# Kernel tuning notes

Hardware: AMD Instinct MI355X
Metric: run time of the kernel (lower is better)

## Reference

```python
import jax, jax.numpy as jnp
import numpy as np

B, T, D, H, L, OUT, FC = 256, 512, 64, 256, 2, 1, 128


def setup_inputs() -> dict:
    key = jax.random.key(0)
    ks = jax.random.split(key, 16)
    s = 1.0 / np.sqrt(H)
    u = lambda k, shape: jax.random.uniform(k, shape, jnp.float32, -s, s)
    return {
        "x": jax.random.normal(ks[0], (B, T, D), jnp.float32),
        # layer 0 LSTM params (PyTorch gate order: i, f, g, o)
        "W_ih0": u(ks[1], (4 * H, D)),
        "W_hh0": u(ks[2], (4 * H, H)),
        "b_ih0": u(ks[3], (4 * H,)),
        "b_hh0": u(ks[4], (4 * H,)),
        # layer 1 LSTM params
        "W_ih1": u(ks[5], (4 * H, H)),
        "W_hh1": u(ks[6], (4 * H, H)),
        "b_ih1": u(ks[7], (4 * H,)),
        "b_hh1": u(ks[8], (4 * H,)),
        # MLP head
        "fc1_w": u(ks[9], (FC, H)),
        "fc1_b": u(ks[10], (FC,)),
        "fc2_w": u(ks[11], (OUT, FC)),
        "fc2_b": u(ks[12], (OUT,)),
    }


def _lstm_layer(x, W_ih, W_hh, b_ih, b_hh):
    # x: [B, T, Din] -> (outputs [B, T, H], final hidden [B, H])
    Bsz = x.shape[0]
    Hh = W_hh.shape[1]
    # precompute input contribution to all gates: [B, T, 4H]
    xg = jnp.einsum("btd,gd->btg", x, W_ih) + b_ih + b_hh

    def step(carry, xt):
        h, c = carry
        g = xt + h @ W_hh.T  # [B, 4H]
        i, f, gg, o = jnp.split(g, 4, axis=-1)
        i = jax.nn.sigmoid(i)
        f = jax.nn.sigmoid(f)
        gg = jnp.tanh(gg)
        o = jax.nn.sigmoid(o)
        c = f * c + i * gg
        h = o * jnp.tanh(c)
        return (h, c), h

    h0 = jnp.zeros((Bsz, Hh), x.dtype)
    (hT, _cT), hs = jax.lax.scan(step, (h0, h0), jnp.swapaxes(xg, 0, 1))
    return jnp.swapaxes(hs, 0, 1), hT


def reference(x, W_ih0, W_hh0, b_ih0, b_hh0, W_ih1, W_hh1, b_ih1, b_hh1,
              fc1_w, fc1_b, fc2_w, fc2_b):
    # eval-mode forward: inter-layer dropout (p=0.2) is a no-op
    y0, h0f = _lstm_layer(x, W_ih0, W_hh0, b_ih0, b_hh0)
    _y1, h1f = _lstm_layer(y0, W_ih1, W_hh1, b_ih1, b_hh1)
    # h_n.view(-1, H): stack per-layer final hidden states -> [L*B, H]
    h_n = jnp.concatenate([h0f, h1f], axis=0)
    out = jax.nn.relu(h_n)
    out = jax.nn.relu(out @ fc1_w.T + fc1_b)
    return out @ fc2_w.T + fc2_b  # [L*B, OUT]
```

## Files before the change

### kernel.cpp

```cpp
#include <hip/hip_runtime.h>

#define Bb 256
#define Tt 512
#define Dd 64
#define Hh 256
#define NP 16
#define HB2 (256 * 256)

typedef unsigned short u16;
typedef _Float16 f16;
typedef __attribute__((ext_vector_type(8))) _Float16 f16x8;
typedef __attribute__((ext_vector_type(4))) _Float16 f16x4;
typedef __attribute__((ext_vector_type(4))) float f32x4;
typedef __attribute__((ext_vector_type(4))) unsigned int u32x4;

__device__ __forceinline__ f16x8 bc8h(u32x4 v) { return __builtin_bit_cast(f16x8, v); }

__device__ __forceinline__ float fsig(float x) {
  x = fminf(fmaxf(x, -30.f), 30.f);
  return 1.f / (1.f + __expf(-x));
}
__device__ __forceinline__ float ftanh(float x) {
  x = fminf(fmaxf(x, -15.f), 15.f);
  float t = __expf(2.f * x);
  return (t - 1.f) / (t + 1.f);
}

__device__ __forceinline__ f16x8 ld16_sc1(const f16* p) {
  f16x8 r;
  asm volatile("global_load_dwordx4 %0, %1, off sc1" : "=v"(r) : "v"(p) : "memory");
  return r;
}
__device__ __forceinline__ void st4_sc1(f16* p, unsigned v) {
  asm volatile("global_store_dword %0, %1, off sc1" : : "v"(p), "v"(v) : "memory");
}

__global__ __launch_bounds__(256) void prep_x(const float* __restrict__ x,
                                              f16* __restrict__ xh) {
  int i = blockIdx.x * blockDim.x + threadIdx.x;
  const int n4 = Bb * Tt * Dd / 4;
  if (i >= n4) return;
  f32x4 v = ((const f32x4*)x)[i];
  f16x4 o;
#pragma unroll
  for (int j = 0; j < 4; ++j) o[j] = (f16)v[j];
  ((f16x4*)xh)[i] = o;
}

__global__ __launch_bounds__(256) void prep_w(
    const float* __restrict__ wih0, const float* __restrict__ whh0,
    const float* __restrict__ bih0, const float* __restrict__ bhh0,
    const float* __restrict__ wih1, const float* __restrict__ whh1,
    const float* __restrict__ bih1, const float* __restrict__ bhh1,
    f16* __restrict__ wfrag, float* __restrict__ bias0s, float* __restrict__ bias1s) {
  int tid = blockIdx.x * blockDim.x + threadIdx.x;
  int np = gridDim.x * blockDim.x;
  const int tot = 16 * 8 * 32 * 512;
  for (int u = tid; u < tot; u += np) {
    int e = u & 7, l = (u >> 3) & 63;
    int f = (u >> 9) & 31;
    int wv = (u >> 14) & 7;
    int p = u >> 17;
    int g = wv & 3;
    int grow = g * 256 + p * 16 + (l & 15);
    int klane = (l >> 4) * 8 + e;
    float w = 0.f;
    if (wv < 4) {
      if (f < 4)       w = wih0[grow * 64 + (f >> 1) * 32 + klane];
      else if (f < 20) w = whh0[grow * 256 + ((f - 4) >> 1) * 32 + klane];
    } else {
      if (f < 16)      w = wih1[grow * 256 + (f >> 1) * 32 + klane];
      else             w = whh1[grow * 256 + ((f - 16) >> 1) * 32 + klane];
    }
    f16 hi = (f16)w;
    wfrag[u] = (f & 1) ? (f16)((w - (float)hi) * 2048.0f) : hi;
  }
  for (int u = tid; u < 1024; u += np) {
    bias0s[u] = bih0[u] + bhh0[u];
    bias1s[u] = bih1[u] + bhh1[u];
  }
}

#define MF(A, B, C) __builtin_amdgcn_mfma_f32_16x16x32_f16(A, B, C, 0, 0, 0)

__global__ __launch_bounds__(512, 2) void lstm_persist(
    const f16* __restrict__ xh, const f16* __restrict__ wfrag,
    const float* __restrict__ bias0s, const float* __restrict__ bias1s,
    f16* h0, f16* h1, unsigned* flags) {
  const int p = blockIdx.x & 15, grp = blockIdx.x >> 4;
  const int tid = threadIdx.x;
  const int wv = tid >> 6, lane = tid & 63;
  const int lr = lane & 15, lk = lane >> 4;
  const int g = wv & 3;
  const bool isL1 = wv >= 4;
  const float LOSCALE = 1.0f / 2048.0f;

  __shared__ float gbuf[2][4][16][16];
  __shared__ u32x4 hbuf[2][16][32];

  f16x8 wf[32];
  {
    const u32x4* wp = (const u32x4*)wfrag + ((size_t)(p * 8 + wv) * 32) * 64 + lane;
#pragma unroll
    for (int f = 0; f < 20; ++f) wf[f] = bc8h(wp[(size_t)f * 64]);
    if (isL1) {
#pragma unroll
      for (int f = 20; f < 32; ++f) wf[f] = bc8h(wp[(size_t)f * 64]);
    }
  }
  const float bias = (isL1 ? bias1s : bias0s)[g * 256 + p * 16 + lr];

  float c0 = 0.f, c1 = 0.f;
  const int hrow = grp * 16 + lr;
  const f16* xbase = xh + (size_t)hrow * Tt * Dd + lk * 8;
  const f16* hsrcbase = ((wv < 4) ? h0 : h1) + (size_t)grp * 4096;
  const int hlsel = wv >> 2;

  for (int k = 0; k <= Tt; ++k) {
    f32x4 a = (f32x4){bias, bias, bias, bias};
    f32x4 b = (f32x4){0.f, 0.f, 0.f, 0.f};
    if (!isL1 && k < Tt) {
      const u32x4* xp = (const u32x4*)(xbase + (size_t)k * Dd);
      f16x8 xf0 = bc8h(xp[0]);
      f16x8 xf1 = bc8h(xp[4]);
      a = MF(xf0, wf[0], a);
      b = MF(xf0, wf[1], b);
      a = MF(xf1, wf[2], a);
      b = MF(xf1, wf[3], b);
    }

    if (wv == 0) {
      bool ready = false;
      while (!ready) {
        unsigned v = 0xFFFFFFFFu;
        if (lane < NP)
          v = __hip_atomic_load(&flags[grp * NP + lane], __ATOMIC_RELAXED,
                                __HIP_MEMORY_SCOPE_AGENT);
        ready = !__any(v < (unsigned)k);
        if (!ready) __builtin_amdgcn_s_sleep(1);
      }
    }
    asm volatile("" ::: "memory");
    __syncthreads();

    const int par = (k - 1) & 1;

    {
      const f16* src = hsrcbase + (size_t)par * HB2;
      const int j0 = (wv & 3) * 2;
      const f16* p0 = src + j0 * 512 + lane * 8;
      f16x8 s0 = ld16_sc1(p0);
      f16x8 s1 = ld16_sc1(p0 + 512);
      asm volatile("s_waitcnt vmcnt(0)" ::: "memory");
      const int r0 = j0 * 2 + (lane >> 5);
      const int c = lane & 31;
      hbuf[hlsel][r0][c ^ (r0 & 7)] = __builtin_bit_cast(u32x4, s0);
      hbuf[hlsel][r0 + 2][c ^ ((r0 + 2) & 7)] = __builtin_bit_cast(u32x4, s1);
    }
    __syncthreads();

    f16x8 A0[8], A1[8];
#pragma unroll
    for (int kt = 0; kt < 8; ++kt)
      A0[kt] = __builtin_bit_cast(f16x8, hbuf[0][lr][(kt * 4 + lk) ^ (lr & 7)]);
    if (isL1) {
#pragma unroll
      for (int kt = 0; kt < 8; ++kt)
        A1[kt] = __builtin_bit_cast(f16x8, hbuf[1][lr][(kt * 4 + lk) ^ (lr & 7)]);
    }

    if (!isL1) {
      if (k < Tt) {
#pragma unroll
        for (int kt = 0; kt < 8; ++kt) {
          a = MF(A0[kt], wf[4 + 2 * kt], a);
          b = MF(A0[kt], wf[5 + 2 * kt], b);
        }
        a += b * LOSCALE;
#pragma unroll
        for (int r = 0; r < 4; ++r) gbuf[0][g][lk * 4 + r][lr] = a[r];
      }
    } else if (k >= 1) {
#pragma unroll
      for (int kt = 0; kt < 8; ++kt) {
        a = MF(A0[kt], wf[2 * kt], a);
        b = MF(A0[kt], wf[2 * kt + 1], b);
      }
#pragma unroll
      for (int kt = 0; kt < 8; ++kt) {
        a = MF(A1[kt], wf[16 + 2 * kt], a);
        b = MF(A1[kt], wf[17 + 2 * kt], b);
      }
      a += b * LOSCALE;
#pragma unroll
      for (int r = 0; r < 4; ++r) gbuf[1][g][lk * 4 + r][lr] = a[r];
    }
    __syncthreads();

    {
      const bool upd = ((wv & 2) == 0) && (isL1 ? (k >= 1) : (k < Tt));
      if (upd) {
        const int L = isL1 ? 1 : 0;
        int id0 = (wv & 1) * 128 + lane * 2;
        int row = id0 >> 4, col = id0 & 15;
        float iv = fsig(gbuf[L][0][row][col]);
        float fv = fsig(gbuf[L][1][row][col]);
        float gv = ftanh(gbuf[L][2][row][col]);
        float ov = fsig(gbuf[L][3][row][col]);
        c0 = fv * c0 + iv * gv;
        float ha = ov * ftanh(c0);
        iv = fsig(gbuf[L][0][row][col + 1]);
        fv = fsig(gbuf[L][1][row][col + 1]);
        gv = ftanh(gbuf[L][2][row][col + 1]);
        ov = fsig(gbuf[L][3][row][col + 1]);
        c1 = fv * c1 + iv * gv;
        float hb = ov * ftanh(c1);
        f16 fa = (f16)ha, fb = (f16)hb;
        unsigned pack = (unsigned)__builtin_bit_cast(u16, fa) |
                        ((unsigned)__builtin_bit_cast(u16, fb) << 16);
        f16* Ho = (isL1 ? h1 : h0) + (size_t)(k & 1) * HB2 +
                  (grp * 16 + row) * 256 + p * 16 + col;
        st4_sc1(Ho, pack);
      }
    }
    asm volatile("s_waitcnt vmcnt(0)" ::: "memory");
    __syncthreads();
    if (tid == 0)
      __hip_atomic_store(&flags[grp * NP + p], (unsigned)(k + 1), __ATOMIC_RELAXED,
                         __HIP_MEMORY_SCOPE_AGENT);
  }
}

__global__ __launch_bounds__(128) void head_kernel(
    const f16* __restrict__ h0f, const f16* __restrict__ h1f,
    const float* __restrict__ fc1w, const float* __restrict__ fc1b,
    const float* __restrict__ fc2w, const float* __restrict__ fc2b,
    float* __restrict__ out) {
  int r = blockIdx.x;
  const f16* hh = (r < 256) ? (h0f + r * Hh) : (h1f + (r - 256) * Hh);
  __shared__ float v[Hh];
  int tid = threadIdx.x;
  for (int i = tid; i < Hh; i += 128)
    v[i] = fmaxf((float)hh[i], 0.f);
  __syncthreads();
  float s = fc1b[tid];
#pragma unroll 8
  for (int i = 0; i < Hh; ++i) s += fc1w[tid * Hh + i] * v[i];
  s = fmaxf(s, 0.f) * fc2w[tid];
#pragma unroll
  for (int off = 32; off; off >>= 1) s += __shfl_down(s, off);
  __shared__ float red[2];
  if ((tid & 63) == 0) red[tid >> 6] = s;
  __syncthreads();
  if (tid == 0) out[r] = red[0] + red[1] + fc2b[0];
}

extern "C" void kernel_launch(void* const* d_in, const int* in_sizes, int n_in,
                              void* d_out, int out_size, void* d_ws, size_t ws_size,
                              hipStream_t stream) {
  (void)in_sizes; (void)n_in; (void)out_size; (void)ws_size;
  const float* x    = (const float*)d_in[0];
  const float* wih0 = (const float*)d_in[1];
  const float* whh0 = (const float*)d_in[2];
  const float* bih0 = (const float*)d_in[3];
  const float* bhh0 = (const float*)d_in[4];
  const float* wih1 = (const float*)d_in[5];
  const float* whh1 = (const float*)d_in[6];
  const float* bih1 = (const float*)d_in[7];
  const float* bhh1 = (const float*)d_in[8];
  const float* fc1w = (const float*)d_in[9];
  const float* fc1b = (const float*)d_in[10];
  const float* fc2w = (const float*)d_in[11];
  const float* fc2b = (const float*)d_in[12];

  char* ws = (char*)d_ws;
  size_t off = 0;
  f16* xh = (f16*)(ws + off); off += (size_t)Bb * Tt * Dd * 2;
  f16* wfrag = (f16*)(ws + off); off += (size_t)16 * 8 * 32 * 512 * 2;
  float* bias0s = (float*)(ws + off); off += 4096;
  float* bias1s = (float*)(ws + off); off += 4096;
  char* zbase = ws + off;
  f16* h0 = (f16*)(ws + off); off += (size_t)2 * HB2 * 2;
  f16* h1 = (f16*)(ws + off); off += (size_t)2 * HB2 * 2;
  unsigned* flags = (unsigned*)(ws + off); off += 1024;
  size_t zbytes = (size_t)((ws + off) - zbase);

  hipMemsetAsync(zbase, 0, zbytes, stream);
  prep_x<<<Bb * Tt * Dd / 4 / 256, 256, 0, stream>>>(x, xh);
  prep_w<<<512, 256, 0, stream>>>(wih0, whh0, bih0, bhh0, wih1, whh1, bih1, bhh1,
                                  wfrag, bias0s, bias1s);
  lstm_persist<<<256, 512, 0, stream>>>(xh, wfrag, bias0s, bias1s, h0, h1, flags);
  head_kernel<<<512, 128, 0, stream>>>(h0 + HB2, h1, fc1w, fc1b, fc2w, fc2b,
                                       (float*)d_out);
}
```

Before: 1.775 ms.

## Probe XCD co-location and use non-coherent hidden-state exchange when safe

Blocks are remapped so the 16 workgroups of a batch group are meant to land on the same XCD. At startup a probe checks whether plain stores become visible through sc0 loads among peers. If every peer sees the probe, the kernel uses plain stores and sc0 loads for the per-step hidden-state exchange instead of sc1 (device-coherent) accesses, to cut the latency of each recurrent step. The hidden buffers grow from 2 to 4 slots, which adds slack between reuse of a slot. The cost is added startup synchronisation and reliance on dispatch placement, with a fallback to the old coherent path.

```diff
diff --git a/kernel.cpp b/kernel.cpp
--- a/kernel.cpp
+++ b/kernel.cpp
@@ -31,8 +31,28 @@
   asm volatile("global_load_dwordx4 %0, %1, off sc1" : "=v"(r) : "v"(p) : "memory");
   return r;
 }
+__device__ __forceinline__ f16x8 ld16_sc0(const f16* p) {
+  f16x8 r;
+  asm volatile("global_load_dwordx4 %0, %1, off sc0" : "=v"(r) : "v"(p) : "memory");
+  return r;
+}
 __device__ __forceinline__ void st4_sc1(f16* p, unsigned v) {
   asm volatile("global_store_dword %0, %1, off sc1" : : "v"(p), "v"(v) : "memory");
+}
+__device__ __forceinline__ void st4_plain(f16* p, unsigned v) {
+  asm volatile("global_store_dword %0, %1, off" : : "v"(p), "v"(v) : "memory");
+}
+__device__ __forceinline__ void st4u_plain(unsigned* p, unsigned v) {
+  asm volatile("global_store_dword %0, %1, off" : : "v"(p), "v"(v) : "memory");
+}
+__device__ __forceinline__ void st4u_sc1(unsigned* p, unsigned v) {
+  asm volatile("global_store_dword %0, %1, off sc1" : : "v"(p), "v"(v) : "memory");
+}
+__device__ __forceinline__ unsigned ld4_sc0(const unsigned* p) {
+  unsigned r;
+  asm volatile("global_load_dword %0, %1, off sc0\n\ts_waitcnt vmcnt(0)"
+               : "=v"(r) : "v"(p) : "memory");
+  return r;
 }
 
 __global__ __launch_bounds__(256) void prep_x(const float* __restrict__ x,
@@ -86,8 +106,10 @@
 __global__ __launch_bounds__(512, 2) void lstm_persist(
     const f16* __restrict__ xh, const f16* __restrict__ wfrag,
     const float* __restrict__ bias0s, const float* __restrict__ bias1s,
-    f16* h0, f16* h1, unsigned* flags) {
-  const int p = blockIdx.x & 15, grp = blockIdx.x >> 4;
+    f16* h0, f16* h1, unsigned* flags, unsigned* probe, unsigned* verdict) {
+  const int bid = blockIdx.x;
+  const int p = (bid >> 3) & 15;
+  const int grp = (bid & 7) * 2 + (bid >> 7);
   const int tid = threadIdx.x;
   const int wv = tid >> 6, lane = tid & 63;
   const int lr = lane & 15, lk = lane >> 4;
@@ -96,7 +118,8 @@
   const float LOSCALE = 1.0f / 2048.0f;
 
   __shared__ float gbuf[2][4][16][16];
-  __shared__ u32x4 hbuf[2][16][32];
+  __shared__ u32x4 hbuf[2][16][36];
+  __shared__ unsigned s_fast;
 
   f16x8 wf[32];
   {
@@ -109,6 +132,52 @@
     }
   }
   const float bias = (isL1 ? bias1s : bias0s)[g * 256 + p * 16 + lr];
+
+  if (tid < 256) {
+    int lsel = tid >> 7;
+    int d = tid & 127;
+    int row = d >> 3, cp = d & 7;
+    f16* base = lsel ? h1 : (h0 + (size_t)3 * HB2);
+    unsigned* w = (unsigned*)(base + (size_t)(grp * 16 + row) * 256 + p * 16) + cp;
+    st4u_plain(w, 0u);
+    st4u_sc1(w, 0u);
+  }
+  asm volatile("s_waitcnt vmcnt(0)" ::: "memory");
+  __syncthreads();
+
+  if (wv == 0) {
+    if (lane == 0) {
+      st4u_plain(&probe[grp * NP + p], (unsigned)(p + 1));
+      asm volatile("s_waitcnt vmcnt(0)" ::: "memory");
+    }
+    bool seen = (lane >= NP);
+    bool ok;
+    int it = 0;
+    while (true) {
+      if (!seen) {
+        unsigned got = ld4_sc0(&probe[grp * NP + lane]);
+        if (got == (unsigned)(lane + 1)) seen = true;
+      }
+      if (__all(seen)) { ok = true; break; }
+      if (++it > 768) { ok = false; break; }
+      __builtin_amdgcn_s_sleep(2);
+    }
+    if (lane == 0)
+      __hip_atomic_store(&verdict[grp * NP + p], ok ? 1u : 2u, __ATOMIC_RELAXED,
+                         __HIP_MEMORY_SCOPE_AGENT);
+    unsigned v;
+    while (true) {
+      v = 1u;
+      if (lane < NP)
+        v = __hip_atomic_load(&verdict[grp * NP + lane], __ATOMIC_RELAXED,
+                              __HIP_MEMORY_SCOPE_AGENT);
+      if (!__any(v == 0u)) break;
+      __builtin_amdgcn_s_sleep(2);
+    }
+    if (lane == 0) s_fast = __any(v != 1u) ? 0u : 1u;
+  }
+  __syncthreads();
+  const bool fast = (s_fast != 0u);
 
   float c0 = 0.f, c1 = 0.f;
   const int hrow = grp * 16 + lr;
@@ -143,14 +212,20 @@
     asm volatile("" ::: "memory");
     __syncthreads();
 
-    const int par = (k - 1) & 1;
+    const int par = (k - 1) & 3;
 
     {
       const f16* src = hsrcbase + (size_t)par * HB2;
       const int j0 = (wv & 3) * 2;
       const f16* p0 = src + j0 * 512 + lane * 8;
-      f16x8 s0 = ld16_sc1(p0);
-      f16x8 s1 = ld16_sc1(p0 + 512);
+      f16x8 s0, s1;
+      if (fast) {
+        s0 = ld16_sc0(p0);
+        s1 = ld16_sc0(p0 + 512);
+      } else {
+        s0 = ld16_sc1(p0);
+        s1 = ld16_sc1(p0 + 512);
+      }
       asm volatile("s_waitcnt vmcnt(0)" ::: "memory");
       const int r0 = j0 * 2 + (lane >> 5);
       const int c = lane & 31;
@@ -218,9 +293,10 @@
         f16 fa = (f16)ha, fb = (f16)hb;
         unsigned pack = (unsigned)__builtin_bit_cast(u16, fa) |
                         ((unsigned)__builtin_bit_cast(u16, fb) << 16);
-        f16* Ho = (isL1 ? h1 : h0) + (size_t)(k & 1) * HB2 +
+        f16* Ho = (isL1 ? h1 : h0) + (size_t)(k & 3) * HB2 +
                   (grp * 16 + row) * 256 + p * 16 + col;
-        st4_sc1(Ho, pack);
+        if (fast) st4_plain(Ho, pack);
+        else      st4_sc1(Ho, pack);
       }
     }
     asm volatile("s_waitcnt vmcnt(0)" ::: "memory");
@@ -280,16 +356,19 @@
   float* bias0s = (float*)(ws + off); off += 4096;
   float* bias1s = (float*)(ws + off); off += 4096;
   char* zbase = ws + off;
-  f16* h0 = (f16*)(ws + off); off += (size_t)2 * HB2 * 2;
-  f16* h1 = (f16*)(ws + off); off += (size_t)2 * HB2 * 2;
+  f16* h0 = (f16*)(ws + off); off += (size_t)4 * HB2 * 2;
+  f16* h1 = (f16*)(ws + off); off += (size_t)4 * HB2 * 2;
   unsigned* flags = (unsigned*)(ws + off); off += 1024;
+  unsigned* probe = (unsigned*)(ws + off); off += 1024;
+  unsigned* verdict = (unsigned*)(ws + off); off += 1024;
   size_t zbytes = (size_t)((ws + off) - zbase);
 
   hipMemsetAsync(zbase, 0, zbytes, stream);
   prep_x<<<Bb * Tt * Dd / 4 / 256, 256, 0, stream>>>(x, xh);
   prep_w<<<512, 256, 0, stream>>>(wih0, whh0, bih0, bhh0, wih1, whh1, bih1, bhh1,
                                   wfrag, bias0s, bias1s);
-  lstm_persist<<<256, 512, 0, stream>>>(xh, wfrag, bias0s, bias1s, h0, h1, flags);
-  head_kernel<<<512, 128, 0, stream>>>(h0 + HB2, h1, fc1w, fc1b, fc2w, fc2b,
-                                       (float*)d_out);
-}
+  lstm_persist<<<256, 512, 0, stream>>>(xh, wfrag, bias0s, bias1s, h0, h1, flags,
+                                        probe, verdict);
+  head_kernel<<<512, 128, 0, stream>>>(h0 + (size_t)3 * HB2, h1, fc1w, fc1b,
+                                       fc2w, fc2b, (float*)d_out);
+}
```

Result: faster. 1.720 ms (-3.1%).
